# Optimization experiments

Hardware: AMD Instinct MI355X
Metric: run time of the kernel (lower is better)

## Reference

```python
import jax, jax.numpy as jnp
import numpy as np

N = 51200      # total nodes
G = 256        # graphs in batch
NPG = 200      # nodes per graph
E = 409600     # intra-graph edges
EPG = E // G
F_IN, HID, HEADS, NCLS = 768, 128, 4, 2


def setup_inputs() -> dict:
    key = jax.random.key(0)
    ks = jax.random.split(key, 20)
    x = jax.random.normal(ks[0], (N, F_IN), jnp.float32)
    # edges strictly inside each graph, no self-loops (PyG batching semantics)
    gid = jnp.arange(E, dtype=jnp.int32) // EPG
    sl = jax.random.randint(ks[1], (E,), 0, NPG, dtype=jnp.int32)
    off = jax.random.randint(ks[2], (E,), 1, NPG, dtype=jnp.int32)
    dl = (sl + off) % NPG
    edge_index = jnp.stack([gid * NPG + sl, gid * NPG + dl])
    batch = jnp.arange(N, dtype=jnp.int32) // NPG

    def glorot(k, shape, fan_in):
        return jax.random.normal(k, shape, jnp.float32) * np.float32(1.0 / np.sqrt(fan_in))

    return {
        'x': x, 'edge_index': edge_index, 'batch': batch,
        'W1': glorot(ks[3], (F_IN, HEADS * HID), F_IN),
        'a_src1': glorot(ks[4], (HEADS, HID), HID),
        'a_dst1': glorot(ks[5], (HEADS, HID), HID),
        'b1': jnp.zeros((HEADS * HID,), jnp.float32),
        'W2': glorot(ks[6], (HEADS * HID, HID), HEADS * HID),
        'a_src2': glorot(ks[7], (1, HID), HID),
        'a_dst2': glorot(ks[8], (1, HID), HID),
        'b2': jnp.zeros((HID,), jnp.float32),
        'Wc': glorot(ks[9], (HID, 2), HID),
        'bc': jnp.zeros((2,), jnp.float32),
        'Wf1': glorot(ks[10], (HID, HID), HID),
        'bf1': jnp.zeros((HID,), jnp.float32),
        'Wf2': glorot(ks[11], (HID, NCLS), HID),
        'bf2': jnp.zeros((NCLS,), jnp.float32),
    }


def _segment_softmax(logits, seg, num):
    m = jax.ops.segment_max(logits, seg, num_segments=num)
    e = jnp.exp(logits - m[seg])
    s = jax.ops.segment_sum(e, seg, num_segments=num)
    return e / (s[seg] + 1e-16)


def _gat(x, src, dst, W, a_s, a_d, b, n):
    # PyG GATConv, eval mode (attention dropout off), self-loops already in src/dst
    H, C = a_s.shape
    h = (x @ W).reshape(n, H, C)                       # [n,H,C]
    a_src = (h * a_s).sum(-1)                          # [n,H]
    a_dst = (h * a_d).sum(-1)
    logits = jax.nn.leaky_relu(a_src[src] + a_dst[dst], 0.2)  # [Etot,H]
    alpha = _segment_softmax(logits, dst, n)
    out = jax.ops.segment_sum(h[src] * alpha[:, :, None], dst, num_segments=n)
    return out.reshape(n, H * C) + b


def reference(x, edge_index, batch, W1, a_src1, a_dst1, b1, W2, a_src2, a_dst2, b2,
              Wc, bc, Wf1, bf1, Wf2, bf2):
    src0, dst0 = edge_index[0], edge_index[1]
    loop = jnp.arange(N, dtype=src0.dtype)
    src = jnp.concatenate([src0, loop])
    dst = jnp.concatenate([dst0, loop])

    h1 = jax.nn.relu(_gat(x, src, dst, W1, a_src1, a_dst1, b1, N))     # [N,512]
    h2 = jax.nn.relu(_gat(h1, src, dst, W2, a_src2, a_dst2, b2, N))    # [N,128]

    S = jax.nn.softmax(h2 @ Wc + bc, axis=1)                           # [N,2]

    # aggregate(): per-graph S^T A S via per-edge outer products (A from original edges)
    eg = batch[src0]
    outer = S[src0][:, :, None] * S[dst0][:, None, :]                  # [E,2,2]
    agg = jax.ops.segment_sum(outer, eg, num_segments=G)               # [G,2,2]
    rnorm = jnp.clip(jnp.abs(agg).sum(axis=2, keepdims=True), 1e-5, None)  # F.normalize p=1 dim=1
    nadj = agg / rnorm
    diag = jnp.diagonal(nadj, axis1=1, axis2=2)                        # [G,2]
    aggregate_loss = jnp.mean(jnp.mean((diag - 1.0) ** 2, axis=1))     # MSE vs ones, averaged over graphs

    # subgraph embedding: first row of S_g^T x_g per graph
    sub = jax.ops.segment_sum(S[:, 0:1] * h2, batch, num_segments=G)   # [G,128]

    out = jax.nn.relu(sub @ Wf1 + bf1)                                 # eval: dropout off
    out = out @ Wf2 + bf2                                              # [G,2]
    return out, aggregate_loss
```

## Files before the change

### kernel.cpp

```cpp
#include <hip/hip_runtime.h>
#include <hip/hip_bf16.h>
#include <cstdint>

#define N_NODES 51200
#define N_GRAPH 256
#define NPG     200
#define N_EDGE  409600
#define EPG     1600
#define F_IN    768
#define HID     128
#define HEADS   4
#define HC      512

typedef __attribute__((ext_vector_type(8))) short short8;
typedef __attribute__((ext_vector_type(4))) float floatx4;

constexpr size_t OFF_H1B    = 0;
constexpr size_t OFF_H2B    = OFF_H1B + (size_t)N_NODES * HC * 2;
constexpr size_t OFF_H2F    = OFF_H2B + (size_t)N_NODES * HID * 2;
constexpr size_t OFF_WT1    = OFF_H2F + (size_t)N_NODES * HID * 4;
constexpr size_t OFF_WT2    = OFF_WT1 + (size_t)HC * F_IN * 2;
constexpr size_t OFF_S      = OFF_WT2 + (size_t)HID * HC * 2;
constexpr size_t OFF_AGG    = OFF_S + (size_t)N_NODES * 2 * 4;
constexpr size_t OFF_SUB    = OFF_AGG + (size_t)N_GRAPH * 4 * 4;

__device__ __forceinline__ float leaky(float x) { return x >= 0.0f ? x : 0.2f * x; }

__device__ __forceinline__ unsigned short f2bf(float f) {
    unsigned int u = __float_as_uint(f);
    u += 0x7fffu + ((u >> 16) & 1u);
    return (unsigned short)(u >> 16);
}
__device__ __forceinline__ float bflo(int p) { return __uint_as_float((unsigned)p << 16); }
__device__ __forceinline__ float bfhi(int p) { return __uint_as_float((unsigned)p & 0xffff0000u); }

__device__ __forceinline__ void gl_lds16(const void* g, void* l) {
    __builtin_amdgcn_global_load_lds(
        (__attribute__((address_space(1))) void*)(g),
        (__attribute__((address_space(3))) void*)(l),
        16, 0, 0);
}

__global__ __launch_bounds__(256)
void transpose_cvt_kernel(const float* __restrict__ W, short* __restrict__ Wt,
                          int K, int Nn)
{
    int idx = blockIdx.x * 256 + threadIdx.x;
    if (idx >= K * Nn) return;
    int k = idx / Nn, n = idx % Nn;
    Wt[(size_t)n * K + k] = (short)f2bf(W[idx]);
}

template <bool A_BF16>
__global__ __launch_bounds__(256)
void gemm_mfma_kernel(const void* __restrict__ Av, const short* __restrict__ Bt,
                      unsigned short* __restrict__ C, int M, int Nn, int K)
{
    __shared__ __align__(16) short Ablob[4096];
    __shared__ __align__(16) short Bblob[4096];
    const int tid = threadIdx.x;
    const int w = tid >> 6, l = tid & 63;
    const int m0 = blockIdx.x * 128, n0 = blockIdx.y * 128;
    const int wr = w >> 1, wc = w & 1;

    floatx4 acc[4][4];
#pragma unroll
    for (int i = 0; i < 4; ++i)
#pragma unroll
        for (int j = 0; j < 4; ++j) acc[i][j] = (floatx4)0.0f;

    const short* bgp = Bt + (size_t)(n0 + (w * 2) * 16 + (l & 15)) * K + ((l >> 4) * 8);

    const float* Af = (const float*)Av;
    const short* Ab = (const short*)Av;
    const int r = tid >> 1, hh = tid & 1;
    const float* arow = Af + (size_t)(m0 + r) * K + hh * 16;
    const short* agp = Ab + (size_t)(m0 + (w * 2) * 16 + (l & 15)) * K + ((l >> 4) * 8);

    float4 pf0, pf1, pf2, pf3;
    if constexpr (!A_BF16) {
        pf0 = *(const float4*)(arow + 0);
        pf1 = *(const float4*)(arow + 4);
        pf2 = *(const float4*)(arow + 8);
        pf3 = *(const float4*)(arow + 12);
    }

    for (int k0 = 0; k0 < K; k0 += 32) {
        __syncthreads();
        if constexpr (A_BF16) {
            gl_lds16(agp + k0,          &Ablob[(w * 2) * 512]);
            gl_lds16(agp + 16 * K + k0, &Ablob[(w * 2 + 1) * 512]);
        } else {
            unsigned short us[16];
            us[0]=f2bf(pf0.x); us[1]=f2bf(pf0.y); us[2]=f2bf(pf0.z); us[3]=f2bf(pf0.w);
            us[4]=f2bf(pf1.x); us[5]=f2bf(pf1.y); us[6]=f2bf(pf1.z); us[7]=f2bf(pf1.w);
            us[8]=f2bf(pf2.x); us[9]=f2bf(pf2.y); us[10]=f2bf(pf2.z); us[11]=f2bf(pf2.w);
            us[12]=f2bf(pf3.x); us[13]=f2bf(pf3.y); us[14]=f2bf(pf3.z); us[15]=f2bf(pf3.w);
            const int o = (r >> 4) * 512 + (2 * hh) * 128 + (r & 15) * 8;
            short8 v0, v1;
#pragma unroll
            for (int j = 0; j < 8; ++j) { v0[j] = (short)us[j]; v1[j] = (short)us[8 + j]; }
            *(short8*)&Ablob[o]       = v0;
            *(short8*)&Ablob[o + 128] = v1;
        }
        gl_lds16(bgp + k0,          &Bblob[(w * 2) * 512]);
        gl_lds16(bgp + 16 * K + k0, &Bblob[(w * 2 + 1) * 512]);
        __syncthreads();

        if constexpr (!A_BF16) {
            if (k0 + 32 < K) {
                pf0 = *(const float4*)(arow + k0 + 32);
                pf1 = *(const float4*)(arow + k0 + 36);
                pf2 = *(const float4*)(arow + k0 + 40);
                pf3 = *(const float4*)(arow + k0 + 44);
            }
        }

        short8 af[4], bfr[4];
#pragma unroll
        for (int mi = 0; mi < 4; ++mi)
            af[mi] = *(const short8*)&Ablob[(wr * 4 + mi) * 512 + l * 8];
#pragma unroll
        for (int ni = 0; ni < 4; ++ni)
            bfr[ni] = *(const short8*)&Bblob[(wc * 4 + ni) * 512 + l * 8];
#pragma unroll
        for (int mi = 0; mi < 4; ++mi)
#pragma unroll
            for (int ni = 0; ni < 4; ++ni)
                acc[mi][ni] = __builtin_amdgcn_mfma_f32_16x16x32_bf16(
                    af[mi], bfr[ni], acc[mi][ni], 0, 0, 0);
    }

    const int lr = (l >> 4) * 4, lc = l & 15;
#pragma unroll
    for (int mi = 0; mi < 4; ++mi)
#pragma unroll
        for (int ni = 0; ni < 4; ++ni) {
            const size_t base = (size_t)(m0 + wr * 64 + mi * 16 + lr) * Nn
                              + (n0 + wc * 64 + ni * 16 + lc);
#pragma unroll
            for (int rr = 0; rr < 4; ++rr)
                C[base + (size_t)rr * Nn] = f2bf(acc[mi][ni][rr]);
        }
}

__global__ __launch_bounds__(256)
void gat1_kernel(const unsigned short* __restrict__ H, const int* __restrict__ src0,
                 const int* __restrict__ dst0, const float* __restrict__ a_s,
                 const float* __restrict__ a_d, const float* __restrict__ b1,
                 unsigned short* __restrict__ out)
{
    const int g = blockIdx.x, h = blockIdx.y;
    __shared__ int   s_feat[NPG * 64];
    __shared__ float s_as[NPG], s_ad[NPG], s_m[NPG], s_inv[NPG];
    __shared__ int   s_row[NPG + 1];
    __shared__ int   s_cnt[NPG], s_fill[NPG];
    __shared__ int   s_scan[256];
    __shared__ float s_w[EPG];
    __shared__ short s_esrc[EPG], s_edst[EPG], s_srcl[EPG], s_dstl[EPG];
    const int tid = threadIdx.x, w = tid >> 6, l = tid & 63;
    const int gbase = g * NPG;

    for (int flat = tid; flat < NPG * 16; flat += 256) {
        int row = flat >> 4, q = flat & 15;
        uint4 v = *(const uint4*)(H + (size_t)(gbase + row) * HC + h * HID + q * 8);
        *(uint4*)&s_feat[row * 64 + q * 4] = v;
    }
    for (int j = tid; j < EPG; j += 256) {
        s_esrc[j] = (short)(src0[g * EPG + j] - gbase);
        s_edst[j] = (short)(dst0[g * EPG + j] - gbase);
    }
    if (tid < NPG) s_cnt[tid] = 0;
    __syncthreads();

    for (int j = tid; j < EPG; j += 256)
        atomicAdd(&s_cnt[(int)s_edst[j]], 1);
    const float2 av = ((const float2*)(a_s + h * HID))[l];
    const float2 dv = ((const float2*)(a_d + h * HID))[l];
    for (int nl = w; nl < NPG; nl += 4) {
        int pk = s_feat[nl * 64 + l];
        float f0 = bflo(pk), f1 = bfhi(pk);
        float ss = f0 * av.x + f1 * av.y;
        float sd = f0 * dv.x + f1 * dv.y;
#pragma unroll
        for (int off = 1; off < 64; off <<= 1) {
            ss += __shfl_xor(ss, off);
            sd += __shfl_xor(sd, off);
        }
        if (l == 0) { s_as[nl] = ss; s_ad[nl] = sd; }
    }
    __syncthreads();

    {
        int v = (tid < NPG) ? s_cnt[tid] : 0;
        s_scan[tid] = v;
        __syncthreads();
        for (int off = 1; off < 256; off <<= 1) {
            int u = (tid >= off) ? s_scan[tid - off] : 0;
            __syncthreads();
            s_scan[tid] += u;
            __syncthreads();
        }
        if (tid < NPG) s_row[tid + 1] = s_scan[tid];
        if (tid == 0) s_row[0] = 0;
        __syncthreads();
        if (tid < NPG) s_fill[tid] = s_row[tid];
    }
    __syncthreads();

    for (int j = tid; j < EPG; j += 256) {
        int dg = (int)s_edst[j];
        int p = atomicAdd(&s_fill[dg], 1);
        s_srcl[p] = s_esrc[j];
        s_dstl[p] = (short)dg;
    }
    __syncthreads();

    for (int j = tid; j < EPG; j += 256)
        s_w[j] = leaky(s_as[(int)s_srcl[j]] + s_ad[(int)s_dstl[j]]);
    __syncthreads();

    if (tid < NPG) {
        float m = leaky(s_as[tid] + s_ad[tid]);
        int r0 = s_row[tid], r1 = s_row[tid + 1];
        for (int j = r0; j < r1; ++j) m = fmaxf(m, s_w[j]);
        s_m[tid] = m;
    }
    __syncthreads();

    for (int j = tid; j < EPG; j += 256)
        s_w[j] = __expf(s_w[j] - s_m[(int)s_dstl[j]]);
    __syncthreads();

    if (tid < NPG) {
        float rs = __expf(leaky(s_as[tid] + s_ad[tid]) - s_m[tid]);
        int r0 = s_row[tid], r1 = s_row[tid + 1];
        for (int j = r0; j < r1; ++j) rs += s_w[j];
        s_inv[tid] = 1.0f / (rs + 1e-16f);
    }
    __syncthreads();

    const float2 bv = ((const float2*)(b1 + h * HID))[l];
    for (int nl = w; nl < NPG; nl += 4) {
        const int r0 = s_row[nl], r1 = s_row[nl + 1];
        const float wself = __expf(leaky(s_as[nl] + s_ad[nl]) - s_m[nl]);
        int spk = s_feat[nl * 64 + l];
        float a0 = wself * bflo(spk), a1 = wself * bfhi(spk);
        float c0 = 0.0f, c1 = 0.0f;
        int j = r0;
        for (; j + 1 < r1; j += 2) {
            float w0 = s_w[j], w1 = s_w[j + 1];
            int p0 = s_feat[(int)s_srcl[j] * 64 + l];
            int p1 = s_feat[(int)s_srcl[j + 1] * 64 + l];
            a0 += w0 * bflo(p0); a1 += w0 * bfhi(p0);
            c0 += w1 * bflo(p1); c1 += w1 * bfhi(p1);
        }
        if (j < r1) {
            float w0 = s_w[j];
            int p0 = s_feat[(int)s_srcl[j] * 64 + l];
            a0 += w0 * bflo(p0); a1 += w0 * bfhi(p0);
        }
        const float inv = s_inv[nl];
        float o0 = (a0 + c0) * inv + bv.x;
        float o1 = (a1 + c1) * inv + bv.y;
        unsigned int st = (unsigned int)f2bf(fmaxf(o0, 0.0f))
                        | ((unsigned int)f2bf(fmaxf(o1, 0.0f)) << 16);
        *(unsigned int*)&out[(size_t)(gbase + nl) * HC + h * HID + 2 * l] = st;
    }
}

__global__ __launch_bounds__(256)
void gat2_kernel(const unsigned short* __restrict__ H, const int* __restrict__ src0,
                 const int* __restrict__ dst0, const float* __restrict__ a_s,
                 const float* __restrict__ a_d, const float* __restrict__ b2,
                 const float* __restrict__ Wc, const float* __restrict__ bc,
                 float* __restrict__ h2, float* __restrict__ S)
{
    const int g = blockIdx.x;
    __shared__ int   s_feat[NPG * 64];
    __shared__ float s_as[NPG], s_ad[NPG], s_m[NPG], s_inv[NPG];
    __shared__ int   s_row[NPG + 1];
    __shared__ int   s_cnt[NPG], s_fill[NPG];
    __shared__ int   s_scan[256];
    __shared__ float s_w[EPG];
    __shared__ short s_esrc[EPG], s_edst[EPG], s_srcl[EPG], s_dstl[EPG];
    const int tid = threadIdx.x, w = tid >> 6, l = tid & 63;
    const int gbase = g * NPG;

    for (int flat = tid; flat < NPG * 16; flat += 256) {
        int row = flat >> 4, q = flat & 15;
        uint4 v = *(const uint4*)(H + (size_t)(gbase + row) * HID + q * 8);
        *(uint4*)&s_feat[row * 64 + q * 4] = v;
    }
    for (int j = tid; j < EPG; j += 256) {
        s_esrc[j] = (short)(src0[g * EPG + j] - gbase);
        s_edst[j] = (short)(dst0[g * EPG + j] - gbase);
    }
    if (tid < NPG) s_cnt[tid] = 0;
    __syncthreads();

    for (int j = tid; j < EPG; j += 256)
        atomicAdd(&s_cnt[(int)s_edst[j]], 1);
    const float2 av = ((const float2*)a_s)[l];
    const float2 dv = ((const float2*)a_d)[l];
    for (int nl = w; nl < NPG; nl += 4) {
        int pk = s_feat[nl * 64 + l];
        float f0 = bflo(pk), f1 = bfhi(pk);
        float ss = f0 * av.x + f1 * av.y;
        float sd = f0 * dv.x + f1 * dv.y;
#pragma unroll
        for (int off = 1; off < 64; off <<= 1) {
            ss += __shfl_xor(ss, off);
            sd += __shfl_xor(sd, off);
        }
        if (l == 0) { s_as[nl] = ss; s_ad[nl] = sd; }
    }
    __syncthreads();

    {
        int v = (tid < NPG) ? s_cnt[tid] : 0;
        s_scan[tid] = v;
        __syncthreads();
        for (int off = 1; off < 256; off <<= 1) {
            int u = (tid >= off) ? s_scan[tid - off] : 0;
            __syncthreads();
            s_scan[tid] += u;
            __syncthreads();
        }
        if (tid < NPG) s_row[tid + 1] = s_scan[tid];
        if (tid == 0) s_row[0] = 0;
        __syncthreads();
        if (tid < NPG) s_fill[tid] = s_row[tid];
    }
    __syncthreads();

    for (int j = tid; j < EPG; j += 256) {
        int dg = (int)s_edst[j];
        int p = atomicAdd(&s_fill[dg], 1);
        s_srcl[p] = s_esrc[j];
        s_dstl[p] = (short)dg;
    }
    __syncthreads();

    for (int j = tid; j < EPG; j += 256)
        s_w[j] = leaky(s_as[(int)s_srcl[j]] + s_ad[(int)s_dstl[j]]);
    __syncthreads();

    if (tid < NPG) {
        float m = leaky(s_as[tid] + s_ad[tid]);
        int r0 = s_row[tid], r1 = s_row[tid + 1];
        for (int j = r0; j < r1; ++j) m = fmaxf(m, s_w[j]);
        s_m[tid] = m;
    }
    __syncthreads();

    for (int j = tid; j < EPG; j += 256)
        s_w[j] = __expf(s_w[j] - s_m[(int)s_dstl[j]]);
    __syncthreads();

    if (tid < NPG) {
        float rs = __expf(leaky(s_as[tid] + s_ad[tid]) - s_m[tid]);
        int r0 = s_row[tid], r1 = s_row[tid + 1];
        for (int j = r0; j < r1; ++j) rs += s_w[j];
        s_inv[tid] = 1.0f / (rs + 1e-16f);
    }
    __syncthreads();

    const float2 bv = ((const float2*)b2)[l];
    const float4 wcv = ((const float4*)Wc)[l];
    const float bc0 = bc[0], bc1 = bc[1];
    for (int nl = w; nl < NPG; nl += 4) {
        const int r0 = s_row[nl], r1 = s_row[nl + 1];
        const float wself = __expf(leaky(s_as[nl] + s_ad[nl]) - s_m[nl]);
        int spk = s_feat[nl * 64 + l];
        float a0 = wself * bflo(spk), a1 = wself * bfhi(spk);
        float c0 = 0.0f, c1 = 0.0f;
        int j = r0;
        for (; j + 1 < r1; j += 2) {
            float w0 = s_w[j], w1 = s_w[j + 1];
            int p0 = s_feat[(int)s_srcl[j] * 64 + l];
            int p1 = s_feat[(int)s_srcl[j + 1] * 64 + l];
            a0 += w0 * bflo(p0); a1 += w0 * bfhi(p0);
            c0 += w1 * bflo(p1); c1 += w1 * bfhi(p1);
        }
        if (j < r1) {
            float w0 = s_w[j];
            int p0 = s_feat[(int)s_srcl[j] * 64 + l];
            a0 += w0 * bflo(p0); a1 += w0 * bfhi(p0);
        }
        const float inv = s_inv[nl];
        float o0 = fmaxf((a0 + c0) * inv + bv.x, 0.0f);
        float o1 = fmaxf((a1 + c1) * inv + bv.y, 0.0f);
        *(float2*)&h2[(size_t)(gbase + nl) * HID + 2 * l] = make_float2(o0, o1);
        float z0 = o0 * wcv.x + o1 * wcv.z;
        float z1 = o0 * wcv.y + o1 * wcv.w;
#pragma unroll
        for (int off = 1; off < 64; off <<= 1) {
            z0 += __shfl_xor(z0, off);
            z1 += __shfl_xor(z1, off);
        }
        if (l == 0) {
            z0 += bc0; z1 += bc1;
            float mm = fmaxf(z0, z1);
            float e0 = __expf(z0 - mm), e1 = __expf(z1 - mm);
            float is = 1.0f / (e0 + e1);
            *(float2*)&S[(size_t)(gbase + nl) * 2] = make_float2(e0 * is, e1 * is);
        }
    }
}

__global__ __launch_bounds__(256)
void agg_kernel(const int* __restrict__ src0, const int* __restrict__ dst0,
                const float* __restrict__ S, float* __restrict__ agg)
{
    const int g = blockIdx.x, tid = threadIdx.x;
    float a00 = 0, a01 = 0, a10 = 0, a11 = 0;
    for (int e = g*EPG + tid; e < (g + 1)*EPG; e += 256) {
        int s = src0[e], d = dst0[e];
        float s0 = S[s*2], s1 = S[s*2 + 1];
        float d0 = S[d*2], d1 = S[d*2 + 1];
        a00 += s0*d0; a01 += s0*d1; a10 += s1*d0; a11 += s1*d1;
    }
    for (int off = 32; off > 0; off >>= 1) {
        a00 += __shfl_down(a00, off); a01 += __shfl_down(a01, off);
        a10 += __shfl_down(a10, off); a11 += __shfl_down(a11, off);
    }
    __shared__ float sred[4][4];
    if ((tid & 63) == 0) {
        int w = tid >> 6;
        sred[w][0] = a00; sred[w][1] = a01; sred[w][2] = a10; sred[w][3] = a11;
    }
    __syncthreads();
    if (tid == 0) {
        agg[g*4 + 0] = sred[0][0] + sred[1][0] + sred[2][0] + sred[3][0];
        agg[g*4 + 1] = sred[0][1] + sred[1][1] + sred[2][1] + sred[3][1];
        agg[g*4 + 2] = sred[0][2] + sred[1][2] + sred[2][2] + sred[3][2];
        agg[g*4 + 3] = sred[0][3] + sred[1][3] + sred[2][3] + sred[3][3];
    }
}

__global__ __launch_bounds__(256)
void loss_kernel(const float* __restrict__ agg, float* __restrict__ out_loss)
{
    int tid = threadIdx.x;
    float a00 = agg[tid*4 + 0], a01 = agg[tid*4 + 1];
    float a10 = agg[tid*4 + 2], a11 = agg[tid*4 + 3];
    float rn0 = fmaxf(fabsf(a00) + fabsf(a01), 1e-5f);
    float rn1 = fmaxf(fabsf(a10) + fabsf(a11), 1e-5f);
    float d0 = a00 / rn0 - 1.0f, d1 = a11 / rn1 - 1.0f;
    float contrib = 0.5f * (d0*d0 + d1*d1);
    for (int off = 32; off > 0; off >>= 1) contrib += __shfl_down(contrib, off);
    __shared__ float sred[4];
    if ((tid & 63) == 0) sred[tid >> 6] = contrib;
    __syncthreads();
    if (tid == 0)
        out_loss[0] = (sred[0] + sred[1] + sred[2] + sred[3]) * (1.0f / N_GRAPH);
}

__global__ __launch_bounds__(128)
void sub_kernel(const float* __restrict__ S, const float* __restrict__ h2,
                float* __restrict__ sub)
{
    const int g = blockIdx.x, c = threadIdx.x;
    const float* Sg = S + (size_t)g * NPG * 2;
    const float* hg = h2 + (size_t)g * NPG * HID;
    float acc = 0.0f;
    for (int i = 0; i < NPG; ++i)
        acc += Sg[i*2] * hg[(size_t)i*HID + c];
    sub[g*HID + c] = acc;
}

__global__ __launch_bounds__(128)
void final_kernel(const float* __restrict__ sub, const float* __restrict__ Wf1,
                  const float* __restrict__ bf1, const float* __restrict__ Wf2,
                  const float* __restrict__ bf2, float* __restrict__ out)
{
    __shared__ float s_sub[128];
    __shared__ float s_fc[128];
    const int g = blockIdx.x, t = threadIdx.x;
    s_sub[t] = sub[g*HID + t];
    __syncthreads();
    float acc = bf1[t];
    for (int c = 0; c < 128; ++c)
        acc += s_sub[c] * Wf1[c*128 + t];
    s_fc[t] = fmaxf(acc, 0.0f);
    __syncthreads();
    if (t < 2) {
        float z = bf2[t];
        for (int j = 0; j < 128; ++j) z += s_fc[j] * Wf2[j*2 + t];
        out[g*2 + t] = z;
    }
}

extern "C" void kernel_launch(void* const* d_in, const int* in_sizes, int n_in,
                              void* d_out, int out_size, void* d_ws, size_t ws_size,
                              hipStream_t stream)
{
    const float* x   = (const float*)d_in[0];
    const int*   ei  = (const int*)d_in[1];
    const float* W1  = (const float*)d_in[3];
    const float* as1 = (const float*)d_in[4];
    const float* ad1 = (const float*)d_in[5];
    const float* b1  = (const float*)d_in[6];
    const float* W2  = (const float*)d_in[7];
    const float* as2 = (const float*)d_in[8];
    const float* ad2 = (const float*)d_in[9];
    const float* b2  = (const float*)d_in[10];
    const float* Wc  = (const float*)d_in[11];
    const float* bc  = (const float*)d_in[12];
    const float* Wf1 = (const float*)d_in[13];
    const float* bf1 = (const float*)d_in[14];
    const float* Wf2 = (const float*)d_in[15];
    const float* bf2 = (const float*)d_in[16];
    const int* src0 = ei;
    const int* dst0 = ei + N_EDGE;

    char* ws = (char*)d_ws;
    unsigned short* H1b = (unsigned short*)(ws + OFF_H1B);
    unsigned short* H2b = (unsigned short*)(ws + OFF_H2B);
    float* h2    = (float*)(ws + OFF_H2F);
    short* Wt1   = (short*)(ws + OFF_WT1);
    short* Wt2   = (short*)(ws + OFF_WT2);
    float* Sbuf  = (float*)(ws + OFF_S);
    float* aggb  = (float*)(ws + OFF_AGG);
    float* subb  = (float*)(ws + OFF_SUB);
    float* out   = (float*)d_out;

    transpose_cvt_kernel<<<(F_IN*HC + 255)/256, 256, 0, stream>>>(W1, Wt1, F_IN, HC);
    transpose_cvt_kernel<<<(HC*HID + 255)/256, 256, 0, stream>>>(W2, Wt2, HC, HID);

    gemm_mfma_kernel<false><<<dim3(N_NODES/128, HC/128), 256, 0, stream>>>(
        x, Wt1, H1b, N_NODES, HC, F_IN);

    gat1_kernel<<<dim3(N_GRAPH, HEADS), 256, 0, stream>>>(
        H1b, src0, dst0, as1, ad1, b1, H1b);

    gemm_mfma_kernel<true><<<dim3(N_NODES/128, HID/128), 256, 0, stream>>>(
        H1b, Wt2, H2b, N_NODES, HID, HC);

    gat2_kernel<<<N_GRAPH, 256, 0, stream>>>(
        H2b, src0, dst0, as2, ad2, b2, Wc, bc, h2, Sbuf);

    agg_kernel<<<N_GRAPH, 256, 0, stream>>>(src0, dst0, Sbuf, aggb);
    loss_kernel<<<1, 256, 0, stream>>>(aggb, out + N_GRAPH*2);

    sub_kernel<<<N_GRAPH, 128, 0, stream>>>(Sbuf, h2, subb);
    final_kernel<<<N_GRAPH, 128, 0, stream>>>(subb, Wf1, bf1, Wf2, bf2, out);

    (void)in_sizes; (void)n_in; (void)out_size; (void)ws_size;
}
```

Measured before the change: 613.1 us.

## Pack edge data into int2 LDS records and widen GAT blocks to 512 threads

Both GAT kernels now pack each edge's local src/dst into one 16-bit word and store the CSR-sorted weight and packed index together in one int2 LDS array. This replaces four short arrays and a separate weight array, and reuses s_scan as the fill cursor. Blocks grow from 256 to 512 threads (8 waves per graph), and the aggregation loop is unrolled by 4 so more LDS loads are in flight. The packing assumes fewer than 256 nodes per graph, and the scan needs extra guards for threads at or above 256.

```diff
diff --git a/kernel.cpp b/kernel.cpp
--- a/kernel.cpp
+++ b/kernel.cpp
@@ -144,7 +144,7 @@
         }
 }
 
-__global__ __launch_bounds__(256)
+__global__ __launch_bounds__(512)
 void gat1_kernel(const unsigned short* __restrict__ H, const int* __restrict__ src0,
                  const int* __restrict__ dst0, const float* __restrict__ a_s,
                  const float* __restrict__ a_d, const float* __restrict__ b1,
@@ -154,30 +154,31 @@
     __shared__ int   s_feat[NPG * 64];
     __shared__ float s_as[NPG], s_ad[NPG], s_m[NPG], s_inv[NPG];
     __shared__ int   s_row[NPG + 1];
-    __shared__ int   s_cnt[NPG], s_fill[NPG];
+    __shared__ int   s_cnt[NPG];
     __shared__ int   s_scan[256];
-    __shared__ float s_w[EPG];
-    __shared__ short s_esrc[EPG], s_edst[EPG], s_srcl[EPG], s_dstl[EPG];
+    __shared__ unsigned short s_eraw[EPG];
+    __shared__ int2  s_wc[EPG];
     const int tid = threadIdx.x, w = tid >> 6, l = tid & 63;
     const int gbase = g * NPG;
 
-    for (int flat = tid; flat < NPG * 16; flat += 256) {
+    for (int flat = tid; flat < NPG * 16; flat += 512) {
         int row = flat >> 4, q = flat & 15;
         uint4 v = *(const uint4*)(H + (size_t)(gbase + row) * HC + h * HID + q * 8);
         *(uint4*)&s_feat[row * 64 + q * 4] = v;
     }
-    for (int j = tid; j < EPG; j += 256) {
-        s_esrc[j] = (short)(src0[g * EPG + j] - gbase);
-        s_edst[j] = (short)(dst0[g * EPG + j] - gbase);
+    for (int j = tid; j < EPG; j += 512) {
+        int s = src0[g * EPG + j] - gbase;
+        int d = dst0[g * EPG + j] - gbase;
+        s_eraw[j] = (unsigned short)(s | (d << 8));
     }
     if (tid < NPG) s_cnt[tid] = 0;
     __syncthreads();
 
-    for (int j = tid; j < EPG; j += 256)
-        atomicAdd(&s_cnt[(int)s_edst[j]], 1);
+    for (int j = tid; j < EPG; j += 512)
+        atomicAdd(&s_cnt[s_eraw[j] >> 8], 1);
     const float2 av = ((const float2*)(a_s + h * HID))[l];
     const float2 dv = ((const float2*)(a_d + h * HID))[l];
-    for (int nl = w; nl < NPG; nl += 4) {
+    for (int nl = w; nl < NPG; nl += 8) {
         int pk = s_feat[nl * 64 + l];
         float f0 = bflo(pk), f1 = bfhi(pk);
         float ss = f0 * av.x + f1 * av.y;
@@ -193,71 +194,81 @@
 
     {
         int v = (tid < NPG) ? s_cnt[tid] : 0;
-        s_scan[tid] = v;
+        if (tid < 256) s_scan[tid] = v;
         __syncthreads();
         for (int off = 1; off < 256; off <<= 1) {
-            int u = (tid >= off) ? s_scan[tid - off] : 0;
+            int u = (tid >= off && tid < 256) ? s_scan[tid - off] : 0;
             __syncthreads();
-            s_scan[tid] += u;
+            if (tid < 256) s_scan[tid] += u;
             __syncthreads();
         }
         if (tid < NPG) s_row[tid + 1] = s_scan[tid];
         if (tid == 0) s_row[0] = 0;
         __syncthreads();
-        if (tid < NPG) s_fill[tid] = s_row[tid];
-    }
-    __syncthreads();
-
-    for (int j = tid; j < EPG; j += 256) {
-        int dg = (int)s_edst[j];
-        int p = atomicAdd(&s_fill[dg], 1);
-        s_srcl[p] = s_esrc[j];
-        s_dstl[p] = (short)dg;
-    }
-    __syncthreads();
-
-    for (int j = tid; j < EPG; j += 256)
-        s_w[j] = leaky(s_as[(int)s_srcl[j]] + s_ad[(int)s_dstl[j]]);
+        if (tid < NPG) s_scan[tid] = s_row[tid];
+    }
+    __syncthreads();
+
+    for (int j = tid; j < EPG; j += 512) {
+        int pk = s_eraw[j];
+        int p = atomicAdd(&s_scan[pk >> 8], 1);
+        s_wc[p].y = pk;
+    }
+    __syncthreads();
+
+    for (int j = tid; j < EPG; j += 512) {
+        int pk = s_wc[j].y;
+        s_wc[j].x = __float_as_int(leaky(s_as[pk & 255] + s_ad[pk >> 8]));
+    }
     __syncthreads();
 
     if (tid < NPG) {
         float m = leaky(s_as[tid] + s_ad[tid]);
         int r0 = s_row[tid], r1 = s_row[tid + 1];
-        for (int j = r0; j < r1; ++j) m = fmaxf(m, s_w[j]);
+        for (int j = r0; j < r1; ++j) m = fmaxf(m, __int_as_float(s_wc[j].x));
         s_m[tid] = m;
     }
     __syncthreads();
 
-    for (int j = tid; j < EPG; j += 256)
-        s_w[j] = __expf(s_w[j] - s_m[(int)s_dstl[j]]);
+    for (int j = tid; j < EPG; j += 512) {
+        int2 e = s_wc[j];
+        s_wc[j].x = __float_as_int(__expf(__int_as_float(e.x) - s_m[e.y >> 8]));
+    }
     __syncthreads();
 
     if (tid < NPG) {
         float rs = __expf(leaky(s_as[tid] + s_ad[tid]) - s_m[tid]);
         int r0 = s_row[tid], r1 = s_row[tid + 1];
-        for (int j = r0; j < r1; ++j) rs += s_w[j];
+        for (int j = r0; j < r1; ++j) rs += __int_as_float(s_wc[j].x);
         s_inv[tid] = 1.0f / (rs + 1e-16f);
     }
     __syncthreads();
 
     const float2 bv = ((const float2*)(b1 + h * HID))[l];
-    for (int nl = w; nl < NPG; nl += 4) {
+    for (int nl = w; nl < NPG; nl += 8) {
         const int r0 = s_row[nl], r1 = s_row[nl + 1];
         const float wself = __expf(leaky(s_as[nl] + s_ad[nl]) - s_m[nl]);
         int spk = s_feat[nl * 64 + l];
         float a0 = wself * bflo(spk), a1 = wself * bfhi(spk);
         float c0 = 0.0f, c1 = 0.0f;
         int j = r0;
-        for (; j + 1 < r1; j += 2) {
-            float w0 = s_w[j], w1 = s_w[j + 1];
-            int p0 = s_feat[(int)s_srcl[j] * 64 + l];
-            int p1 = s_feat[(int)s_srcl[j + 1] * 64 + l];
+        for (; j + 4 <= r1; j += 4) {
+            int2 e0 = s_wc[j], e1 = s_wc[j + 1], e2 = s_wc[j + 2], e3 = s_wc[j + 3];
+            int p0 = s_feat[(e0.y & 255) * 64 + l];
+            int p1 = s_feat[(e1.y & 255) * 64 + l];
+            int p2 = s_feat[(e2.y & 255) * 64 + l];
+            int p3 = s_feat[(e3.y & 255) * 64 + l];
+            float w0 = __int_as_float(e0.x), w1 = __int_as_float(e1.x);
+            float w2 = __int_as_float(e2.x), w3 = __int_as_float(e3.x);
             a0 += w0 * bflo(p0); a1 += w0 * bfhi(p0);
             c0 += w1 * bflo(p1); c1 += w1 * bfhi(p1);
-        }
-        if (j < r1) {
-            float w0 = s_w[j];
-            int p0 = s_feat[(int)s_srcl[j] * 64 + l];
+            a0 += w2 * bflo(p2); a1 += w2 * bfhi(p2);
+            c0 += w3 * bflo(p3); c1 += w3 * bfhi(p3);
+        }
+        for (; j < r1; ++j) {
+            int2 e0 = s_wc[j];
+            int p0 = s_feat[(e0.y & 255) * 64 + l];
+            float w0 = __int_as_float(e0.x);
             a0 += w0 * bflo(p0); a1 += w0 * bfhi(p0);
         }
         const float inv = s_inv[nl];
@@ -269,7 +280,7 @@
     }
 }
 
-__global__ __launch_bounds__(256)
+__global__ __launch_bounds__(512)
 void gat2_kernel(const unsigned short* __restrict__ H, const int* __restrict__ src0,
                  const int* __restrict__ dst0, const float* __restrict__ a_s,
                  const float* __restrict__ a_d, const float* __restrict__ b2,
@@ -280,30 +291,31 @@
     __shared__ int   s_feat[NPG * 64];
     __shared__ float s_as[NPG], s_ad[NPG], s_m[NPG], s_inv[NPG];
     __shared__ int   s_row[NPG + 1];
-    __shared__ int   s_cnt[NPG], s_fill[NPG];
+    __shared__ int   s_cnt[NPG];
     __shared__ int   s_scan[256];
-    __shared__ float s_w[EPG];
-    __shared__ short s_esrc[EPG], s_edst[EPG], s_srcl[EPG], s_dstl[EPG];
+    __shared__ unsigned short s_eraw[EPG];
+    __shared__ int2  s_wc[EPG];
     const int tid = threadIdx.x, w = tid >> 6, l = tid & 63;
     const int gbase = g * NPG;
 
-    for (int flat = tid; flat < NPG * 16; flat += 256) {
+    for (int flat = tid; flat < NPG * 16; flat += 512) {
         int row = flat >> 4, q = flat & 15;
         uint4 v = *(const uint4*)(H + (size_t)(gbase + row) * HID + q * 8);
         *(uint4*)&s_feat[row * 64 + q * 4] = v;
     }
-    for (int j = tid; j < EPG; j += 256) {
-        s_esrc[j] = (short)(src0[g * EPG + j] - gbase);
-        s_edst[j] = (short)(dst0[g * EPG + j] - gbase);
+    for (int j = tid; j < EPG; j += 512) {
+        int s = src0[g * EPG + j] - gbase;
+        int d = dst0[g * EPG + j] - gbase;
+        s_eraw[j] = (unsigned short)(s | (d << 8));
     }
     if (tid < NPG) s_cnt[tid] = 0;
     __syncthreads();
 
-    for (int j = tid; j < EPG; j += 256)
-        atomicAdd(&s_cnt[(int)s_edst[j]], 1);
+    for (int j = tid; j < EPG; j += 512)
+        atomicAdd(&s_cnt[s_eraw[j] >> 8], 1);
     const float2 av = ((const float2*)a_s)[l];
     const float2 dv = ((const float2*)a_d)[l];
-    for (int nl = w; nl < NPG; nl += 4) {
+    for (int nl = w; nl < NPG; nl += 8) {
         int pk = s_feat[nl * 64 + l];
         float f0 = bflo(pk), f1 = bfhi(pk);
         float ss = f0 * av.x + f1 * av.y;
@@ -319,49 +331,52 @@
 
     {
         int v = (tid < NPG) ? s_cnt[tid] : 0;
-        s_scan[tid] = v;
+        if (tid < 256) s_scan[tid] = v;
         __syncthreads();
         for (int off = 1; off < 256; off <<= 1) {
-            int u = (tid >= off) ? s_scan[tid - off] : 0;
+            int u = (tid >= off && tid < 256) ? s_scan[tid - off] : 0;
             __syncthreads();
-            s_scan[tid] += u;
+            if (tid < 256) s_scan[tid] += u;
             __syncthreads();
         }
         if (tid < NPG) s_row[tid + 1] = s_scan[tid];
         if (tid == 0) s_row[0] = 0;
         __syncthreads();
-        if (tid < NPG) s_fill[tid] = s_row[tid];
-    }
-    __syncthreads();
-
-    for (int j = tid; j < EPG; j += 256) {
-        int dg = (int)s_edst[j];
-        int p = atomicAdd(&s_fill[dg], 1);
-        s_srcl[p] = s_esrc[j];
-        s_dstl[p] = (short)dg;
-    }
-    __syncthreads();
-
-    for (int j = tid; j < EPG; j += 256)
-        s_w[j] = leaky(s_as[(int)s_srcl[j]] + s_ad[(int)s_dstl[j]]);
+        if (tid < NPG) s_scan[tid] = s_row[tid];
+    }
+    __syncthreads();
+
+    for (int j = tid; j < EPG; j += 512) {
+        int pk = s_eraw[j];
+        int p = atomicAdd(&s_scan[pk >> 8], 1);
+        s_wc[p].y = pk;
+    }
+    __syncthreads();
+
+    for (int j = tid; j < EPG; j += 512) {
+        int pk = s_wc[j].y;
+        s_wc[j].x = __float_as_int(leaky(s_as[pk & 255] + s_ad[pk >> 8]));
+    }
     __syncthreads();
 
     if (tid < NPG) {
         float m = leaky(s_as[tid] + s_ad[tid]);
         int r0 = s_row[tid], r1 = s_row[tid + 1];
-        for (int j = r0; j < r1; ++j) m = fmaxf(m, s_w[j]);
+        for (int j = r0; j < r1; ++j) m = fmaxf(m, __int_as_float(s_wc[j].x));
         s_m[tid] = m;
     }
     __syncthreads();
 
-    for (int j = tid; j < EPG; j += 256)
-        s_w[j] = __expf(s_w[j] - s_m[(int)s_dstl[j]]);
+    for (int j = tid; j < EPG; j += 512) {
+        int2 e = s_wc[j];
+        s_wc[j].x = __float_as_int(__expf(__int_as_float(e.x) - s_m[e.y >> 8]));
+    }
     __syncthreads();
 
     if (tid < NPG) {
         float rs = __expf(leaky(s_as[tid] + s_ad[tid]) - s_m[tid]);
         int r0 = s_row[tid], r1 = s_row[tid + 1];
-        for (int j = r0; j < r1; ++j) rs += s_w[j];
+        for (int j = r0; j < r1; ++j) rs += __int_as_float(s_wc[j].x);
         s_inv[tid] = 1.0f / (rs + 1e-16f);
     }
     __syncthreads();
@@ -369,23 +384,30 @@
     const float2 bv = ((const float2*)b2)[l];
     const float4 wcv = ((const float4*)Wc)[l];
     const float bc0 = bc[0], bc1 = bc[1];
-    for (int nl = w; nl < NPG; nl += 4) {
+    for (int nl = w; nl < NPG; nl += 8) {
         const int r0 = s_row[nl], r1 = s_row[nl + 1];
         const float wself = __expf(leaky(s_as[nl] + s_ad[nl]) - s_m[nl]);
         int spk = s_feat[nl * 64 + l];
         float a0 = wself * bflo(spk), a1 = wself * bfhi(spk);
         float c0 = 0.0f, c1 = 0.0f;
         int j = r0;
-        for (; j + 1 < r1; j += 2) {
-            float w0 = s_w[j], w1 = s_w[j + 1];
-            int p0 = s_feat[(int)s_srcl[j] * 64 + l];
-            int p1 = s_feat[(int)s_srcl[j + 1] * 64 + l];
+        for (; j + 4 <= r1; j += 4) {
+            int2 e0 = s_wc[j], e1 = s_wc[j + 1], e2 = s_wc[j + 2], e3 = s_wc[j + 3];
+            int p0 = s_feat[(e0.y & 255) * 64 + l];
+            int p1 = s_feat[(e1.y & 255) * 64 + l];
+            int p2 = s_feat[(e2.y & 255) * 64 + l];
+            int p3 = s_feat[(e3.y & 255) * 64 + l];
+            float w0 = __int_as_float(e0.x), w1 = __int_as_float(e1.x);
+            float w2 = __int_as_float(e2.x), w3 = __int_as_float(e3.x);
             a0 += w0 * bflo(p0); a1 += w0 * bfhi(p0);
             c0 += w1 * bflo(p1); c1 += w1 * bfhi(p1);
-        }
-        if (j < r1) {
-            float w0 = s_w[j];
-            int p0 = s_feat[(int)s_srcl[j] * 64 + l];
+            a0 += w2 * bflo(p2); a1 += w2 * bfhi(p2);
+            c0 += w3 * bflo(p3); c1 += w3 * bfhi(p3);
+        }
+        for (; j < r1; ++j) {
+            int2 e0 = s_wc[j];
+            int p0 = s_feat[(e0.y & 255) * 64 + l];
+            float w0 = __int_as_float(e0.x);
             a0 += w0 * bflo(p0); a1 += w0 * bfhi(p0);
         }
         const float inv = s_inv[nl];
@@ -532,13 +554,13 @@
     gemm_mfma_kernel<false><<<dim3(N_NODES/128, HC/128), 256, 0, stream>>>(
         x, Wt1, H1b, N_NODES, HC, F_IN);
 
-    gat1_kernel<<<dim3(N_GRAPH, HEADS), 256, 0, stream>>>(
+    gat1_kernel<<<dim3(N_GRAPH, HEADS), 512, 0, stream>>>(
         H1b, src0, dst0, as1, ad1, b1, H1b);
 
     gemm_mfma_kernel<true><<<dim3(N_NODES/128, HID/128), 256, 0, stream>>>(
         H1b, Wt2, H2b, N_NODES, HID, HC);
 
-    gat2_kernel<<<N_GRAPH, 256, 0, stream>>>(
+    gat2_kernel<<<N_GRAPH, 512, 0, stream>>>(
         H2b, src0, dst0, as2, ad2, b2, Wc, bc, h2, Sbuf);
 
     agg_kernel<<<N_GRAPH, 256, 0, stream>>>(src0, dst0, Sbuf, aggb);
```

Result: faster. 520.1 us (-15.2%).
